# Optimization experiments

Hardware: AMD Instinct MI355X
Metric: run time of the kernel (lower is better)

The kernel has to match this reference:

```python
import jax, jax.numpy as jnp
import numpy as np

N_NODES = 50000
N_EDGES = 800000
D = 64  # in_dim = hidden_dim = out_dim


def gcn_conv(x, edge_index, W, b, num_nodes):
    """PyG GCNConv: x' = D^{-1/2} (A + I) D^{-1/2} (x W) + b."""
    h = x @ W  # [N, out]
    # add self-loops
    loop = jnp.arange(num_nodes, dtype=edge_index.dtype)
    row = jnp.concatenate([edge_index[0], loop])  # sources j
    col = jnp.concatenate([edge_index[1], loop])  # targets i
    # symmetric normalization
    ones = jnp.ones(row.shape[0], dtype=h.dtype)
    deg = jax.ops.segment_sum(ones, col, num_segments=num_nodes)
    dinv = jnp.where(deg > 0, jax.lax.rsqrt(deg), 0.0)
    norm = dinv[row] * dinv[col]  # [E+N]
    # gather -> scale -> scatter-add
    msg = h[row] * norm[:, None]
    out = jax.ops.segment_sum(msg, col, num_segments=num_nodes)
    return out + b


def setup_inputs() -> dict:
    key = jax.random.key(0)
    k = jax.random.split(key, 6)
    x = jax.random.normal(k[0], (N_NODES, D), dtype=jnp.float32)
    edge_index = jax.random.randint(k[1], (2, N_EDGES), 0, N_NODES, dtype=jnp.int64)
    s = 1.0 / np.sqrt(D)
    W1 = jax.random.uniform(k[2], (D, D), jnp.float32, -s, s)
    b1 = jnp.zeros((D,), jnp.float32)
    W2 = jax.random.uniform(k[3], (D, D), jnp.float32, -s, s)
    b2 = jnp.zeros((D,), jnp.float32)
    return {"x": x, "edge_index": edge_index, "W1": W1, "b1": b1, "W2": W2, "b2": b2}


def reference(x, edge_index, W1, b1, W2, b2):
    h = gcn_conv(x, edge_index, W1, b1, N_NODES)
    h = jax.nn.relu(h)
    out = gcn_conv(h, edge_index, W2, b2, N_NODES)
    return out
```

## Files before the change

kernel.cpp:

```cpp
#include <hip/hip_runtime.h>
#include <hip/hip_fp16.h>

#define N_NODES 50000
#define N_EDGES 800000
#define D 64
#define CAP 64
#define GEMM1_BLOCKS (N_NODES / 16)
#define FILL_BLOCKS  ((N_EDGES / 2 + 255) / 256)

__device__ __forceinline__ float ldf(float v)  { return v; }
__device__ __forceinline__ float ldf(__half v) { return __half2float(v); }

template<typename InT>
__device__ __forceinline__ void gemm_body(int blk, const InT* __restrict__ X,
                                          const float* __restrict__ W,
                                          __half* __restrict__ H) {
    int tid  = threadIdx.x;
    int lane = tid & 63;
    int wave = tid >> 6;
    float w[64];
    #pragma unroll
    for (int k = 0; k < 64; ++k) w[k] = W[k * 64 + lane];
    int node0 = blk * 16 + wave * 4;
    #pragma unroll
    for (int r = 0; r < 4; ++r) {
        int node = node0 + r;
        float xv = ldf(X[node * 64 + lane]);
        float a0 = 0.f, a1 = 0.f;
        #pragma unroll
        for (int k = 0; k < 64; k += 2) {
            a0 = fmaf(__shfl(xv, k, 64),     w[k],     a0);
            a1 = fmaf(__shfl(xv, k + 1, 64), w[k + 1], a1);
        }
        H[node * 64 + lane] = __float2half(a0 + a1);
    }
}

template<typename InT>
__global__ __launch_bounds__(256)
void gemm_kernel(const InT* __restrict__ X, const float* __restrict__ W,
                 __half* __restrict__ H) {
    gemm_body(blockIdx.x, X, W, H);
}

__global__ __launch_bounds__(256)
void fused_gemm1_fill(const float* __restrict__ X, const float* __restrict__ W,
                      __half* __restrict__ H, const int* __restrict__ row,
                      const int* __restrict__ col, int* __restrict__ cnt,
                      int* __restrict__ srcs) {
    if (blockIdx.x < GEMM1_BLOCKS) {
        gemm_body(blockIdx.x, X, W, H);
    } else {
        int idx = (blockIdx.x - GEMM1_BLOCKS) * 256 + threadIdx.x;
        if (idx < N_EDGES / 2) {
            int2 c2 = ((const int2*)col)[idx];
            int2 r2 = ((const int2*)row)[idx];
            int p0 = atomicAdd(&cnt[c2.x], 1);
            if (p0 < CAP) srcs[c2.x * CAP + p0] = r2.x;
            int p1 = atomicAdd(&cnt[c2.y], 1);
            if (p1 < CAP) srcs[c2.y * CAP + p1] = r2.y;
        }
    }
}

__global__ __launch_bounds__(256)
void dinv_kernel(const int* __restrict__ cnt, float* __restrict__ dinv) {
    int i = blockIdx.x * 256 + threadIdx.x;
    if (i < N_NODES) dinv[i] = rsqrtf((float)(cnt[i] + 1));
}

template<bool RELU, typename OutT>
__global__ __launch_bounds__(256)
void gather_kernel(const __half* __restrict__ H, const int* __restrict__ cnt,
                   const int* __restrict__ srcs, const float* __restrict__ dinv,
                   const float* __restrict__ bias, OutT* __restrict__ out) {
    int tid  = threadIdx.x;
    int lane = tid & 63;
    int node = blockIdx.x * 4 + (tid >> 6);
    float di   = dinv[node];
    float acc0 = di * __half2float(H[node * 64 + lane]);
    float acc1 = 0.f, acc2 = 0.f, acc3 = 0.f;
    int n = min(cnt[node], CAP);
    const int* sp = srcs + node * CAP;
    int s = 0; float w = 0.f;
    if (lane < n) { s = sp[lane]; w = dinv[s]; }
    int nr = (n + 7) & ~7;
    for (int j = 0; j < nr; j += 8) {
        int   s0 = __shfl(s, j + 0, 64), s1 = __shfl(s, j + 1, 64);
        int   s2 = __shfl(s, j + 2, 64), s3 = __shfl(s, j + 3, 64);
        int   s4 = __shfl(s, j + 4, 64), s5 = __shfl(s, j + 5, 64);
        int   s6 = __shfl(s, j + 6, 64), s7 = __shfl(s, j + 7, 64);
        float w0 = __shfl(w, j + 0, 64), w1 = __shfl(w, j + 1, 64);
        float w2 = __shfl(w, j + 2, 64), w3 = __shfl(w, j + 3, 64);
        float w4 = __shfl(w, j + 4, 64), w5 = __shfl(w, j + 5, 64);
        float w6 = __shfl(w, j + 6, 64), w7 = __shfl(w, j + 7, 64);
        float v0 = __half2float(H[s0 * 64 + lane]);
        float v1 = __half2float(H[s1 * 64 + lane]);
        float v2 = __half2float(H[s2 * 64 + lane]);
        float v3 = __half2float(H[s3 * 64 + lane]);
        float v4 = __half2float(H[s4 * 64 + lane]);
        float v5 = __half2float(H[s5 * 64 + lane]);
        float v6 = __half2float(H[s6 * 64 + lane]);
        float v7 = __half2float(H[s7 * 64 + lane]);
        acc0 += w0 * v0 + w4 * v4;
        acc1 += w1 * v1 + w5 * v5;
        acc2 += w2 * v2 + w6 * v6;
        acc3 += w3 * v3 + w7 * v7;
    }
    float res = di * ((acc0 + acc1) + (acc2 + acc3)) + bias[lane];
    if (RELU) res = fmaxf(res, 0.f);
    if constexpr (sizeof(OutT) == 2)
        out[node * 64 + lane] = __float2half(res);
    else
        out[node * 64 + lane] = res;
}

extern "C" void kernel_launch(void* const* d_in, const int* in_sizes, int n_in,
                              void* d_out, int out_size, void* d_ws, size_t ws_size,
                              hipStream_t stream) {
    const float* x   = (const float*)d_in[0];
    const int*   ei  = (const int*)d_in[1];
    const int*   row = ei;
    const int*   col = ei + N_EDGES;
    const float* W1  = (const float*)d_in[2];
    const float* b1  = (const float*)d_in[3];
    const float* W2  = (const float*)d_in[4];
    const float* b2  = (const float*)d_in[5];
    float* out = (float*)d_out;

    char* p = (char*)d_ws;
    __half* h    = (__half*)p; p += (size_t)N_NODES * D * 2;
    __half* g    = (__half*)p; p += (size_t)N_NODES * D * 2;
    int*    cnt  = (int*)p;    p += (size_t)N_NODES * 4;
    float*  dinv = (float*)p;  p += (size_t)N_NODES * 4;
    int*    srcs = (int*)p;    p += (size_t)N_NODES * CAP * 4;

    hipMemsetAsync(cnt, 0, (size_t)N_NODES * 4, stream);

    fused_gemm1_fill<<<GEMM1_BLOCKS + FILL_BLOCKS, 256, 0, stream>>>(
        x, W1, h, row, col, cnt, srcs);
    dinv_kernel<<<(N_NODES + 255) / 256, 256, 0, stream>>>(cnt, dinv);
    gather_kernel<true, __half><<<N_NODES / 4, 256, 0, stream>>>(
        h, cnt, srcs, dinv, b1, g);
    gemm_kernel<__half><<<N_NODES / 16, 256, 0, stream>>>(g, W2, h);
    gather_kernel<false, float><<<N_NODES / 4, 256, 0, stream>>>(
        h, cnt, srcs, dinv, b2, out);
}
```

Baseline: 251.1 us.

## Partition edges per block with LDS atomics and fuse layer-2 GEMM into gather

Replaces global-atomic CSR fill with a partition kernel where each of 125 blocks scans all edges and bins those targeting its 400-node range using shared-memory counters, storing 16-bit source indices. Drops the memset and dinv kernel by recomputing rsqrt from counts in the gather, and fuses the second GEMM into the first gather's epilogue. The partition kernel rereads the full col array 125 times, which adds read bandwidth. Storing sources as unsigned short truncates node indices above 65535; that is only safe because N_NODES is 50000.

```diff
diff --git a/kernel.cpp b/kernel.cpp
--- a/kernel.cpp
+++ b/kernel.cpp
@@ -5,27 +5,54 @@
 #define N_EDGES 800000
 #define D 64
 #define CAP 64
-#define GEMM1_BLOCKS (N_NODES / 16)
-#define FILL_BLOCKS  ((N_EDGES / 2 + 255) / 256)
+#define PBLK 125
+#define NPB  400
 
-__device__ __forceinline__ float ldf(float v)  { return v; }
-__device__ __forceinline__ float ldf(__half v) { return __half2float(v); }
+__global__ __launch_bounds__(1024)
+void partition_kernel(const int* __restrict__ row, const int* __restrict__ col,
+                      int* __restrict__ cnt_g, unsigned short* __restrict__ srcs) {
+    __shared__ int cnt[NPB];
+    int tid = threadIdx.x;
+    int lo  = blockIdx.x * NPB;
+    for (int i = tid; i < NPB; i += 1024) cnt[i] = 0;
+    __syncthreads();
+    const int4* c4 = (const int4*)col;
+    for (int i = tid; i < N_EDGES / 4; i += 1024) {
+        int4 c = c4[i];
+        int dx = c.x - lo, dy = c.y - lo, dz = c.z - lo, dw = c.w - lo;
+        if ((unsigned)dx < NPB) {
+            int p = atomicAdd(&cnt[dx], 1);
+            if (p < CAP) srcs[(size_t)(lo + dx) * CAP + p] = (unsigned short)row[4 * i + 0];
+        }
+        if ((unsigned)dy < NPB) {
+            int p = atomicAdd(&cnt[dy], 1);
+            if (p < CAP) srcs[(size_t)(lo + dy) * CAP + p] = (unsigned short)row[4 * i + 1];
+        }
+        if ((unsigned)dz < NPB) {
+            int p = atomicAdd(&cnt[dz], 1);
+            if (p < CAP) srcs[(size_t)(lo + dz) * CAP + p] = (unsigned short)row[4 * i + 2];
+        }
+        if ((unsigned)dw < NPB) {
+            int p = atomicAdd(&cnt[dw], 1);
+            if (p < CAP) srcs[(size_t)(lo + dw) * CAP + p] = (unsigned short)row[4 * i + 3];
+        }
+    }
+    __syncthreads();
+    for (int i = tid; i < NPB; i += 1024) cnt_g[lo + i] = cnt[i];
+}
 
-template<typename InT>
-__device__ __forceinline__ void gemm_body(int blk, const InT* __restrict__ X,
-                                          const float* __restrict__ W,
-                                          __half* __restrict__ H) {
-    int tid  = threadIdx.x;
-    int lane = tid & 63;
-    int wave = tid >> 6;
+__global__ __launch_bounds__(256)
+void gemm_kernel(const float* __restrict__ X, const float* __restrict__ W,
+                 __half* __restrict__ H) {
+    int tid = threadIdx.x, lane = tid & 63, wv = tid >> 6;
     float w[64];
     #pragma unroll
     for (int k = 0; k < 64; ++k) w[k] = W[k * 64 + lane];
-    int node0 = blk * 16 + wave * 4;
+    int node0 = blockIdx.x * 16 + wv * 4;
     #pragma unroll
     for (int r = 0; r < 4; ++r) {
         int node = node0 + r;
-        float xv = ldf(X[node * 64 + lane]);
+        float xv = X[node * 64 + lane];
         float a0 = 0.f, a1 = 0.f;
         #pragma unroll
         for (int k = 0; k < 64; k += 2) {
@@ -36,54 +63,22 @@
     }
 }
 
-template<typename InT>
-__global__ __launch_bounds__(256)
-void gemm_kernel(const InT* __restrict__ X, const float* __restrict__ W,
-                 __half* __restrict__ H) {
-    gemm_body(blockIdx.x, X, W, H);
-}
-
-__global__ __launch_bounds__(256)
-void fused_gemm1_fill(const float* __restrict__ X, const float* __restrict__ W,
-                      __half* __restrict__ H, const int* __restrict__ row,
-                      const int* __restrict__ col, int* __restrict__ cnt,
-                      int* __restrict__ srcs) {
-    if (blockIdx.x < GEMM1_BLOCKS) {
-        gemm_body(blockIdx.x, X, W, H);
-    } else {
-        int idx = (blockIdx.x - GEMM1_BLOCKS) * 256 + threadIdx.x;
-        if (idx < N_EDGES / 2) {
-            int2 c2 = ((const int2*)col)[idx];
-            int2 r2 = ((const int2*)row)[idx];
-            int p0 = atomicAdd(&cnt[c2.x], 1);
-            if (p0 < CAP) srcs[c2.x * CAP + p0] = r2.x;
-            int p1 = atomicAdd(&cnt[c2.y], 1);
-            if (p1 < CAP) srcs[c2.y * CAP + p1] = r2.y;
-        }
-    }
-}
-
-__global__ __launch_bounds__(256)
-void dinv_kernel(const int* __restrict__ cnt, float* __restrict__ dinv) {
-    int i = blockIdx.x * 256 + threadIdx.x;
-    if (i < N_NODES) dinv[i] = rsqrtf((float)(cnt[i] + 1));
-}
-
-template<bool RELU, typename OutT>
+template<int FUSE>
 __global__ __launch_bounds__(256)
 void gather_kernel(const __half* __restrict__ H, const int* __restrict__ cnt,
-                   const int* __restrict__ srcs, const float* __restrict__ dinv,
-                   const float* __restrict__ bias, OutT* __restrict__ out) {
-    int tid  = threadIdx.x;
-    int lane = tid & 63;
+                   const unsigned short* __restrict__ srcs,
+                   const float* __restrict__ bias, const float* __restrict__ W2,
+                   void* __restrict__ outp) {
+    int tid = threadIdx.x, lane = tid & 63;
     int node = blockIdx.x * 4 + (tid >> 6);
-    float di   = dinv[node];
+    int cn = cnt[node];
+    float di = rsqrtf((float)(cn + 1));
+    int n = min(cn, CAP);
+    const unsigned short* sp = srcs + (size_t)node * CAP;
+    int s = 0; float w = 0.f;
+    if (lane < n) { s = sp[lane]; w = rsqrtf((float)(cnt[s] + 1)); }
     float acc0 = di * __half2float(H[node * 64 + lane]);
     float acc1 = 0.f, acc2 = 0.f, acc3 = 0.f;
-    int n = min(cnt[node], CAP);
-    const int* sp = srcs + node * CAP;
-    int s = 0; float w = 0.f;
-    if (lane < n) { s = sp[lane]; w = dinv[s]; }
     int nr = (n + 7) & ~7;
     for (int j = 0; j < nr; j += 8) {
         int   s0 = __shfl(s, j + 0, 64), s1 = __shfl(s, j + 1, 64);
@@ -107,12 +102,22 @@
         acc2 += w2 * v2 + w6 * v6;
         acc3 += w3 * v3 + w7 * v7;
     }
-    float res = di * ((acc0 + acc1) + (acc2 + acc3)) + bias[lane];
-    if (RELU) res = fmaxf(res, 0.f);
-    if constexpr (sizeof(OutT) == 2)
-        out[node * 64 + lane] = __float2half(res);
-    else
-        out[node * 64 + lane] = res;
+    float gval = di * ((acc0 + acc1) + (acc2 + acc3)) + bias[lane];
+    if constexpr (FUSE) {
+        gval = fmaxf(gval, 0.f);
+        float wc[64];
+        #pragma unroll
+        for (int k = 0; k < 64; ++k) wc[k] = W2[k * 64 + lane];
+        float o0 = 0.f, o1 = 0.f;
+        #pragma unroll
+        for (int k = 0; k < 64; k += 2) {
+            o0 = fmaf(__shfl(gval, k, 64),     wc[k],     o0);
+            o1 = fmaf(__shfl(gval, k + 1, 64), wc[k + 1], o1);
+        }
+        ((__half*)outp)[node * 64 + lane] = __float2half(o0 + o1);
+    } else {
+        ((float*)outp)[node * 64 + lane] = gval;
+    }
 }
 
 extern "C" void kernel_launch(void* const* d_in, const int* in_sizes, int n_in,
@@ -129,20 +134,14 @@
     float* out = (float*)d_out;
 
     char* p = (char*)d_ws;
-    __half* h    = (__half*)p; p += (size_t)N_NODES * D * 2;
-    __half* g    = (__half*)p; p += (size_t)N_NODES * D * 2;
-    int*    cnt  = (int*)p;    p += (size_t)N_NODES * 4;
-    float*  dinv = (float*)p;  p += (size_t)N_NODES * 4;
-    int*    srcs = (int*)p;    p += (size_t)N_NODES * CAP * 4;
+    __half* h   = (__half*)p;  p += (size_t)N_NODES * D * 2;
+    __half* h2  = (__half*)p;  p += (size_t)N_NODES * D * 2;
+    int*    cnt = (int*)p;     p += (size_t)N_NODES * 4;
+    unsigned short* srcs = (unsigned short*)p;
+    p += (size_t)N_NODES * CAP * 2;
 
-    hipMemsetAsync(cnt, 0, (size_t)N_NODES * 4, stream);
-
-    fused_gemm1_fill<<<GEMM1_BLOCKS + FILL_BLOCKS, 256, 0, stream>>>(
-        x, W1, h, row, col, cnt, srcs);
-    dinv_kernel<<<(N_NODES + 255) / 256, 256, 0, stream>>>(cnt, dinv);
-    gather_kernel<true, __half><<<N_NODES / 4, 256, 0, stream>>>(
-        h, cnt, srcs, dinv, b1, g);
-    gemm_kernel<__half><<<N_NODES / 16, 256, 0, stream>>>(g, W2, h);
-    gather_kernel<false, float><<<N_NODES / 4, 256, 0, stream>>>(
-        h, cnt, srcs, dinv, b2, out);
+    partition_kernel<<<PBLK, 1024, 0, stream>>>(row, col, cnt, srcs);
+    gemm_kernel<<<N_NODES / 16, 256, 0, stream>>>(x, W1, h);
+    gather_kernel<1><<<N_NODES / 4, 256, 0, stream>>>(h, cnt, srcs, b1, W2, h2);
+    gather_kernel<0><<<N_NODES / 4, 256, 0, stream>>>(h2, cnt, srcs, b2, nullptr, out);
 }
```

Result: slower. 349.7 us (+39.3%).
